# Performance work log

Hardware: AMD Instinct MI355X
Metric: run time of the kernel (lower is better)

Reference implementation:

```python
import jax, jax.numpy as jnp
import numpy as np

N_ATOMS = 30000
N_PAIRS = 1200000
N_BASIS = 7
N_RADIAL = 5
N_SPECIES = 119
R_MIN = 0.5
R_MAX = 6.0
UNITS = (512, 512)
BOX = 6.0  # Angstrom box edge so many pairs fall inside the cutoff
N_FEAT = 360  # gaussian-moment feature count for n_radial=5

# static triangular index sets (fully symmetric contractions)
_TRI2_I, _TRI2_J = np.triu_indices(N_RADIAL)
_TRI3 = np.array([(i, j, k) for i in range(N_RADIAL)
                  for j in range(i, N_RADIAL)
                  for k in range(j, N_RADIAL)], dtype=np.int32)


def setup_inputs() -> dict:
    key = jax.random.key(0)
    ks = jax.random.split(key, 8)
    R = jax.random.uniform(ks[0], (N_ATOMS, 3), jnp.float32) * BOX
    Z = jax.random.randint(ks[1], (N_ATOMS,), 0, N_SPECIES, dtype=jnp.int32)
    idx = jax.random.randint(ks[2], (2, N_PAIRS), 0, N_ATOMS, dtype=jnp.int32)
    W_radial = jax.random.normal(ks[3], (N_SPECIES, N_SPECIES, N_RADIAL, N_BASIS), jnp.float32) / np.sqrt(N_BASIS)
    w1 = jax.random.normal(ks[4], (N_FEAT, UNITS[0]), jnp.float32) / np.sqrt(N_FEAT)
    b1 = jnp.zeros((UNITS[0],), jnp.float32)
    w2 = jax.random.normal(ks[5], (UNITS[0], UNITS[1]), jnp.float32) / np.sqrt(UNITS[0])
    b2 = jnp.zeros((UNITS[1],), jnp.float32)
    w3 = jax.random.normal(ks[6], (UNITS[1], 1), jnp.float32) / np.sqrt(UNITS[1])
    b3 = jnp.zeros((1,), jnp.float32)
    scale = 2.0 * jnp.ones((N_SPECIES, 1), jnp.float32)
    shift = 1.0 * jnp.ones((N_SPECIES, 1), jnp.float32)
    return dict(R=R, Z=Z, idx=idx, W_radial=W_radial, w1=w1, b1=b1,
                w2=w2, b2=b2, w3=w3, b3=b3, scale=scale, shift=shift)


def _descriptor(R, Z, idx, W_radial):
    idx_i, idx_j = idx[0], idx[1]
    # pairwise displacement (free-space displacement fn)
    dr_vec = R[idx_j] - R[idx_i]                                  # [P,3]
    dr = jnp.sqrt(jnp.sum(dr_vec * dr_vec, axis=-1) + 1e-12)      # [P]
    dn = dr_vec / (dr + 1e-5)[:, None]                            # unit vectors [P,3]

    # gaussian radial basis
    betta = N_BASIS ** 2 / R_MAX ** 2
    rad_norm = (2.0 * betta / np.pi) ** 0.25
    shifts = R_MIN + (R_MAX - R_MIN) / N_BASIS * jnp.arange(N_BASIS, dtype=jnp.float32)
    basis = rad_norm * jnp.exp(-betta * (dr[:, None] - shifts) ** 2)  # [P,B]

    # cosine cutoff and per species-pair embedding of the basis
    cutoff = 0.5 * (jnp.cos(jnp.pi * dr / R_MAX) + 1.0) * (dr < R_MAX)
    coeffs = W_radial[Z[idx_i], Z[idx_j]]                          # [P,K,B] irregular gather
    radial = jnp.einsum('pkb,pb->pk', coeffs, basis)               # [P,K]
    radial = radial * (cutoff / np.sqrt(N_BASIS))[:, None]

    seg = lambda x: jax.ops.segment_sum(x, idx_i, num_segments=N_ATOMS)
    # geometric moments of order 0..3
    m0 = seg(radial)                                               # [A,K]
    m1 = seg(radial[:, :, None] * dn[:, None, :])                  # [A,K,3]
    dn2 = dn[:, :, None] * dn[:, None, :]                          # [P,3,3]
    m2 = seg(radial[:, :, None, None] * dn2[:, None])              # [A,K,3,3]
    dn3 = dn2[:, :, :, None] * dn[:, None, None, :]                # [P,3,3,3]
    m3 = seg(radial[:, :, None, None, None] * dn3[:, None])        # [A,K,3,3,3]

    # gaussian-moment invariant contractions
    c1 = jnp.einsum('ari,asi->ars', m1, m1)
    c2 = jnp.einsum('arij,asij->ars', m2, m2)
    c3 = jnp.einsum('arijk,asijk->ars', m3, m3)
    c4 = jnp.einsum('arij,asik,atjk->arst', m2, m2, m2)
    c5 = jnp.einsum('ari,asj,atij->arst', m1, m1, m2)
    c6 = jnp.einsum('arijk,asijl,atkl->arst', m3, m3, m2)
    c7 = jnp.einsum('arijk,asij,atk->arst', m3, m2, m1)

    A = m0.shape[0]
    gm = jnp.concatenate([
        m0,
        c1[:, _TRI2_I, _TRI2_J],
        c2[:, _TRI2_I, _TRI2_J],
        c3[:, _TRI2_I, _TRI2_J],
        c4[:, _TRI3[:, 0], _TRI3[:, 1], _TRI3[:, 2]],
        c5[:, _TRI2_I, _TRI2_J, :].reshape(A, -1),
        c6[:, _TRI2_I, _TRI2_J, :].reshape(A, -1),
        c7.reshape(A, -1),
    ], axis=-1)                                                    # [A,360]
    return gm


def reference(R, Z, idx, W_radial, w1, b1, w2, b2, w3, b3, scale, shift):
    gm = _descriptor(R, Z, idx, W_radial)
    h = jax.nn.swish(gm @ w1 + b1)
    h = jax.nn.swish(h @ w2 + b2)
    h = h @ w3 + b3                                                # [A,1]
    return scale[Z] * h + shift[Z]
```

## Files before the change

kernel.cpp:

```cpp
#include <hip/hip_runtime.h>

#define NA      30000
#define MPAD    30080
#define NPAIRS  1200000
#define NB      7
#define NK      5
#define NSP     119
#define NFEAT   360
#define KP1     384
#define NU      512
#define WROWH   40
#define MAXSLOT 120
#define PSTRIDE 128
#define NBK     118
#define BCAP    11520
#define PPB     4688
#define NTILE   235

#define BETTA      1.3611111111111112f
#define RADNORM    0.96481348f
#define SHIFT_STEP 0.7857142857142857f
#define PI_OVER_R  0.5235987755982988f
#define INV_SQRT7  0.3779644730092272f
#define RMAXV      6.0f
#define TCOEF      2.138888888888889f

typedef __attribute__((ext_vector_type(8))) short bf16x8;
typedef __attribute__((ext_vector_type(4))) float f32x4;
typedef __attribute__((ext_vector_type(2))) float f32x2;
typedef __attribute__((ext_vector_type(4))) unsigned int u32x4;
typedef _Float16 h16x2 __attribute__((ext_vector_type(2)));

__device__ __forceinline__ unsigned short f2b(float x) {
    unsigned u = __float_as_uint(x);
    unsigned r = u + 0x7FFF + ((u >> 16) & 1);
    return (unsigned short)(r >> 16);
}

__global__ __launch_bounds__(256)
void k_part(const int* __restrict__ idx, const int* __restrict__ Z,
            int* __restrict__ gcur, int* __restrict__ part) {
    __shared__ int hist[NBK];
    __shared__ int base[NBK];
    int tid = threadIdx.x;
    for (int b = tid; b < NBK; b += 256) hist[b] = 0;
    __syncthreads();
    int p0 = blockIdx.x * PPB;
    int p1 = min(p0 + PPB, NPAIRS);
    for (int p = p0 + tid; p < p1; p += 256)
        atomicAdd(&hist[idx[p] >> 8], 1);
    __syncthreads();
    for (int b = tid; b < NBK; b += 256) {
        base[b] = atomicAdd(&gcur[b], hist[b]);
        hist[b] = 0;
    }
    __syncthreads();
    for (int p = p0 + tid; p < p1; p += 256) {
        int i = idx[p];
        int b = i >> 8;
        int j = idx[NPAIRS + p];
        int zj = Z[j];
        int off = base[b] + atomicAdd(&hist[b], 1);
        if (off < BCAP)
            part[b * BCAP + off] = ((i & 255) << 22) | (zj << 15) | j;
    }
}

__global__ __launch_bounds__(256)
void k_csr(const int* __restrict__ part, const int* __restrict__ gcnt,
           int* __restrict__ counts, int* __restrict__ plist) {
    __shared__ int lp[128 * MAXSLOT];
    __shared__ int lc[128];
    int tid = threadIdx.x;
    int lane = tid & 63, wave = tid >> 6;
    int w = blockIdx.x;
    int cb = w >> 1;
    int par = w & 1;
    for (int t = tid; t < 128; t += 256) lc[t] = 0;
    __syncthreads();
    int n = min(gcnt[cb], BCAP);
    for (int e = tid; e < n; e += 256) {
        int v = part[cb * BCAP + e];
        int iloc = v >> 22;
        if ((iloc >> 7) == par) {
            int i7 = iloc & 127;
            int r = atomicAdd(&lc[i7], 1);
            if (r < MAXSLOT) lp[i7 * MAXSLOT + r] = v & 0x3FFFFF;
        }
    }
    __syncthreads();
    for (int t = tid; t < 128; t += 256) {
        int a = w * 128 + t;
        if (a < NA) counts[a] = min(lc[t], MAXSLOT);
    }
    for (int rr = 0; rr < 32; rr++) {
        int row = wave * 32 + rr;
        int a = w * 128 + row;
        if (a < NA) {
            int n_r = min(lc[row], MAXSLOT);
            for (int c = lane; c < n_r; c += 64)
                plist[(size_t)a * PSTRIDE + c] = lp[row * MAXSLOT + c];
        }
    }
}

#define PREP_W   (NSP*NSP*WROWH)
#define PREP_R   NA
#define PREP_W1  (NU*KP1)
#define PREP_W2  (NU*NU)
#define PREP_TOT (PREP_W + PREP_R + PREP_W1 + PREP_W2)
__global__ void k_prep(const float* __restrict__ W, const float* __restrict__ R,
                       const float* __restrict__ w1, const float* __restrict__ w2,
                       unsigned short* __restrict__ Wp, float* __restrict__ Rp,
                       unsigned short* __restrict__ w1T, unsigned short* __restrict__ w2T,
                       int* __restrict__ gcur, float* __restrict__ out) {
    int i = blockIdx.x * blockDim.x + threadIdx.x;
    if (i < 128) gcur[i] = 0;
    if (i < NA) out[i] = 0.f;
    if (i < PREP_W) {
        int row = i / WROWH, e = i - row * WROWH;
        int k = e >> 3, b = e & 7;
        float v = (b < 7) ? W[row * (NK * NB) + k * NB + b] : 0.f;
        ((_Float16*)Wp)[i] = (_Float16)v;
        return;
    }
    i -= PREP_W;
    if (i < PREP_R) {
        f32x4 v = {R[3*i], R[3*i+1], R[3*i+2], 0.f};
        *(f32x4*)&Rp[4*i] = v;
        return;
    }
    i -= PREP_R;
    if (i < PREP_W1) {
        int c = i / KP1, kp = i - c * KP1;
        w1T[i] = (kp < NFEAT) ? f2b(w1[kp * NU + c]) : (unsigned short)0;
        return;
    }
    i -= PREP_W1;
    if (i < PREP_W2) {
        int c = i >> 9, kp = i & 511;
        w2T[i] = f2b(w2[kp * NU + c]);
    }
}

#define LDM(comp) M[(comp) * 65]

__device__ __forceinline__ void do_c5(const float* M, unsigned short* STrow,
                                      int r, int s, int foff) {
    const int S2[3][3] = {{0,1,2},{1,3,4},{2,4,5}};
    float m1r[3], m1q[3];
#pragma unroll
    for (int i = 0; i < 3; i++) m1r[i] = LDM(r*20+1+i);
#pragma unroll
    for (int i = 0; i < 3; i++) m1q[i] = LDM(s*20+1+i);
    float pre[9];
#pragma unroll
    for (int i = 0; i < 3; i++)
#pragma unroll
        for (int j = 0; j < 3; j++) pre[i*3+j] = m1r[i] * m1q[j];
    for (int t = 0; t < 5; t++) {
        float m2t[6];
#pragma unroll
        for (int u = 0; u < 6; u++) m2t[u] = LDM(t*20+4+u);
        float v = 0.f;
#pragma unroll
        for (int i = 0; i < 3; i++)
#pragma unroll
            for (int j = 0; j < 3; j++)
                v += pre[i*3+j] * m2t[S2[i][j]];
        STrow[foff + t] = f2b(v);
    }
}

__device__ __forceinline__ void do_c6(const float* M, unsigned short* STrow,
                                      int r, int s, int foff) {
    const int S2[3][3] = {{0,1,2},{1,3,4},{2,4,5}};
    const int S3[3][3][3] = {
        {{0,1,2},{1,3,4},{2,4,5}},
        {{1,3,4},{3,6,7},{4,7,8}},
        {{2,4,5},{4,7,8},{5,8,9}}
    };
    float m3r[10];
#pragma unroll
    for (int u = 0; u < 10; u++) m3r[u] = LDM(r*20+10+u);
    float m2q[6];
#pragma unroll
    for (int u = 0; u < 6; u++) m2q[u] = LDM(s*20+4+u);
    float U0 = 0.f, U1 = 0.f, U2 = 0.f;
#pragma unroll
    for (int i = 0; i < 3; i++)
#pragma unroll
        for (int j = 0; j < 3; j++) {
            float ww = m2q[S2[i][j]];
            U0 += m3r[S3[i][j][0]] * ww;
            U1 += m3r[S3[i][j][1]] * ww;
            U2 += m3r[S3[i][j][2]] * ww;
        }
    for (int t = 0; t < 5; t++) {
        float v = U0 * LDM(t*20+1) + U1 * LDM(t*20+2) + U2 * LDM(t*20+3);
        STrow[foff + t] = f2b(v);
    }
}

__device__ __forceinline__ void do_c7(const float* M, unsigned short* STrow,
                                      int r, int s, int foff) {
    const int S2[3][3] = {{0,1,2},{1,3,4},{2,4,5}};
    const int S3[3][3][3] = {
        {{0,1,2},{1,3,4},{2,4,5}},
        {{1,3,4},{3,6,7},{4,7,8}},
        {{2,4,5},{4,7,8},{5,8,9}}
    };
    float m3r[10], m3q[10];
#pragma unroll
    for (int u = 0; u < 10; u++) m3r[u] = LDM(r*20+10+u);
#pragma unroll
    for (int u = 0; u < 10; u++) m3q[u] = LDM(s*20+10+u);
    float T[3][3];
#pragma unroll
    for (int k = 0; k < 3; k++)
#pragma unroll
        for (int l = 0; l < 3; l++) {
            float v = 0.f;
#pragma unroll
            for (int i = 0; i < 3; i++)
#pragma unroll
                for (int j = 0; j < 3; j++)
                    v += m3r[S3[i][j][k]] * m3q[S3[i][j][l]];
            T[k][l] = v;
        }
    for (int t = 0; t < 5; t++) {
        float m2t[6];
#pragma unroll
        for (int u = 0; u < 6; u++) m2t[u] = LDM(t*20+4+u);
        float v = 0.f;
#pragma unroll
        for (int k = 0; k < 3; k++)
#pragma unroll
            for (int l = 0; l < 3; l++)
                v += T[k][l] * m2t[S2[k][l]];
        STrow[foff + t] = f2b(v);
    }
}

__global__ __launch_bounds__(512, 2)
void k_momcon(const float* __restrict__ Rp, const int* __restrict__ Z,
              const unsigned short* __restrict__ WpH, const int* __restrict__ counts,
              const int* __restrict__ plist, unsigned short* __restrict__ gmB) {
    __shared__ float MS[100 * 65];
    __shared__ __align__(4) unsigned short ST[64 * 242];
    int tid = threadIdx.x;
    int g = tid >> 3, q = tid & 7;
    int a0 = blockIdx.x * 64;
    int a = a0 + g;

    if (a < NA) {
        f32x4 ri = *(const f32x4*)&Rp[4*a];
        int Zi = Z[a];
        f32x2 acc[50];
#pragma unroll
        for (int u = 0; u < 50; u++) acc[u] = (f32x2){0.f, 0.f};
        int cnt = min(counts[a], MAXSLOT);
        const int* prow = plist + (size_t)a * PSTRIDE;

        const float DCH[6] = {0.14812156f, 0.027590652f, 0.0051393300f,
                              0.00095730500f, 0.00017831700f, 3.3215300e-05f};

        int pk0 = prow[q & 127];
        int pk1 = prow[(q + 8) & 127];
        int j0c = min(pk0 & 0x7FFF, NA - 1);
        f32x4 rj = *(const f32x4*)&Rp[4 * j0c];

        for (int t = q; t < cnt; t += 8) {
            int pk2 = prow[(t + 16) & 127];
            int j1c = min(pk1 & 0x7FFF, NA - 1);
            f32x4 rjn = *(const f32x4*)&Rp[4 * j1c];

            int Zj = (pk0 >> 15) & 0x7F;
            const u32x4* wv = (const u32x4*)(WpH + (size_t)(Zi * NSP + Zj) * WROWH);
            u32x4 wv0 = wv[0], wv1 = wv[1], wv2 = wv[2], wv3 = wv[3], wv4 = wv[4];
            unsigned wu[20];
#pragma unroll
            for (int c = 0; c < 4; c++) {
                wu[c]      = wv0[c];
                wu[4 + c]  = wv1[c];
                wu[8 + c]  = wv2[c];
                wu[12 + c] = wv3[c];
                wu[16 + c] = wv4[c];
            }

            float dx = rj.x - ri.x, dy = rj.y - ri.y, dz = rj.z - ri.z;
            float d2 = dx*dx + dy*dy + dz*dz + 1e-12f;
            float dr = sqrtf(d2);
            float inv = 1.0f / (dr + 1e-5f);
            float nx = dx*inv, ny = dy*inv, nz = dz*inv;

            float t0 = dr - 0.5f;
            float bb[NB];
            bb[0] = RADNORM * __expf(-BETTA * t0 * t0);
            float Tg = __expf(TCOEF * dr);
#pragma unroll
            for (int b = 0; b < 6; b++) bb[b+1] = bb[b] * Tg * DCH[b];

            float cut = (dr < RMAXV) ? 0.5f * (__cosf(PI_OVER_R * dr) + 1.0f) : 0.0f;
            cut *= INV_SQRT7;

            h16x2 bp[4];
            bp[0] = (h16x2){(_Float16)bb[0], (_Float16)bb[1]};
            bp[1] = (h16x2){(_Float16)bb[2], (_Float16)bb[3]};
            bp[2] = (h16x2){(_Float16)bb[4], (_Float16)bb[5]};
            bp[3] = (h16x2){(_Float16)bb[6], (_Float16)0.0f};

            float rad[NK];
#pragma unroll
            for (int k = 0; k < NK; k++) {
                float s = 0.f;
#if __has_builtin(__builtin_amdgcn_fdot2)
#pragma unroll
                for (int c = 0; c < 4; c++)
                    s = __builtin_amdgcn_fdot2(
                        __builtin_bit_cast(h16x2, wu[k*4 + c]), bp[c], s, false);
#else
#pragma unroll
                for (int c = 0; c < 4; c++) {
                    h16x2 w = __builtin_bit_cast(h16x2, wu[k*4 + c]);
                    s += (float)w.x * (float)bp[c].x + (float)w.y * (float)bp[c].y;
                }
#endif
                rad[k] = s * cut;
            }

            float gg[20];
            gg[0] = 1.f; gg[1] = nx; gg[2] = ny; gg[3] = nz;
            gg[4] = nx*nx; gg[5] = nx*ny; gg[6] = nx*nz; gg[7] = ny*ny; gg[8] = ny*nz; gg[9] = nz*nz;
            gg[10] = gg[4]*nx; gg[11] = gg[4]*ny; gg[12] = gg[4]*nz; gg[13] = gg[5]*ny; gg[14] = gg[5]*nz;
            gg[15] = gg[6]*nz; gg[16] = gg[7]*ny; gg[17] = gg[7]*nz; gg[18] = gg[8]*nz; gg[19] = gg[9]*nz;
            f32x2 g2[10];
#pragma unroll
            for (int u = 0; u < 10; u++) g2[u] = (f32x2){gg[2*u], gg[2*u+1]};
#pragma unroll
            for (int k = 0; k < NK; k++) {
                f32x2 rk = (f32x2){rad[k], rad[k]};
#pragma unroll
                for (int u = 0; u < 10; u++)
                    acc[k*10 + u] += rk * g2[u];
            }
            pk0 = pk1; pk1 = pk2; rj = rjn;
        }
#pragma unroll
        for (int u = 0; u < 50; u++) {
            f32x2 v = acc[u];
            double d = __builtin_bit_cast(double, v);
            d = __shfl_xor(d, 1);
            v += __builtin_bit_cast(f32x2, d);
            d = __builtin_bit_cast(double, v);
            d = __shfl_xor(d, 2);
            v += __builtin_bit_cast(f32x2, d);
            d = __builtin_bit_cast(double, v);
            d = __shfl_xor(d, 4);
            v += __builtin_bit_cast(f32x2, d);
            acc[u] = v;
        }
        if (q == 0) {
#pragma unroll
            for (int u = 0; u < 50; u++) {
                MS[(2*u)     * 65 + g] = acc[u].x;
                MS[(2*u + 1) * 65 + g] = acc[u].y;
            }
        }
    }
    __syncthreads();

    int lane = tid & 63, wave = tid >> 6;
    const float* M = MS + lane;
    unsigned short* STrow = ST + lane * 242;

    if (wave == 0) {
        for (int k = 0; k < 5; k++) STrow[k] = f2b(LDM(k * 20));
        int f = 5;
        for (int r = 0; r < 5; r++)
            for (int s = r; s < 5; s++) {
                float v = 0.f;
#pragma unroll
                for (int i = 0; i < 3; i++) v += LDM(r*20+1+i) * LDM(s*20+1+i);
                STrow[f++] = f2b(v);
            }
        const float W2U[6] = {1,2,2,1,2,1};
        for (int r = 0; r < 5; r++)
            for (int s = r; s < 5; s++) {
                float v = 0.f;
#pragma unroll
                for (int u = 0; u < 6; u++) v += W2U[u] * LDM(r*20+4+u) * LDM(s*20+4+u);
                STrow[f++] = f2b(v);
            }
        const float W3U[10] = {1,3,3,3,6,3,1,3,3,1};
        for (int r = 0; r < 5; r++)
            for (int s = r; s < 5; s++) {
                float v = 0.f;
#pragma unroll
                for (int u = 0; u < 10; u++) v += W3U[u] * LDM(r*20+10+u) * LDM(s*20+10+u);
                STrow[f++] = f2b(v);
            }
        do_c7(M, STrow, 3, 4, 160 + 13*5);
        do_c7(M, STrow, 4, 4, 160 + 14*5);
    } else if (wave == 1 || wave == 2) {
        const int S2[3][3] = {{0,1,2},{1,3,4},{2,4,5}};
        int e0 = (wave == 1) ? 0 : 18, e1 = (wave == 1) ? 18 : 35;
        int e = 0;
        for (int r = 0; r < 5; r++)
            for (int s = r; s < 5; s++)
                for (int t = s; t < 5; t++) {
                    if (e >= e0 && e < e1) {
                        float m2r[6], m2q[6], m2t[6];
#pragma unroll
                        for (int u = 0; u < 6; u++) m2r[u] = LDM(r*20+4+u);
#pragma unroll
                        for (int u = 0; u < 6; u++) m2q[u] = LDM(s*20+4+u);
#pragma unroll
                        for (int u = 0; u < 6; u++) m2t[u] = LDM(t*20+4+u);
                        float v = 0.f;
#pragma unroll
                        for (int i = 0; i < 3; i++)
#pragma unroll
                            for (int j = 0; j < 3; j++)
#pragma unroll
                                for (int k = 0; k < 3; k++)
                                    v += m2r[S2[i][j]] * m2q[S2[i][k]] * m2t[S2[j][k]];
                        STrow[50 + e] = f2b(v);
                    }
                    e++;
                }
    } else if (wave == 3) {
        int p = 0;
        for (int r = 0; r < 5; r++)
            for (int s = r; s < 5; s++) {
                if (p < 8) do_c5(M, STrow, r, s, 85 + p*5);
                p++;
            }
        do_c7(M, STrow, 3, 3, 160 + 12*5);
    } else if (wave == 4) {
        int p = 0;
        for (int r = 0; r < 5; r++)
            for (int s = r; s < 5; s++) {
                if (p >= 8) do_c5(M, STrow, r, s, 85 + p*5);
                p++;
            }
        do_c6(M, STrow, 0, 0, 235);
    } else {
        int pc0 = (wave - 5) * 4;
        int p = 0;
        for (int r = 0; r < 5; r++)
            for (int s = r; s < 5; s++) {
                if (p >= pc0 && p < pc0 + 4) do_c7(M, STrow, r, s, 160 + p*5);
                p++;
            }
    }
    __syncthreads();
    for (int e = tid; e < 64 * 120; e += 512) {
        int row = e / 120, c = e - row * 120;
        if (a0 + row < NA)
            *(unsigned int*)&gmB[(size_t)(a0 + row) * KP1 + 2*c] =
                *(const unsigned int*)&ST[row * 242 + 2*c];
    }
    __syncthreads();

    {
        int g0 = 1 + wave * 3;
        for (int gi = 0; gi < 3; gi++) {
            int gr = g0 + gi;
            int r = gr / 5, s = gr - r * 5;
            do_c6(M, STrow, r, s, 235 + gr*5 - 240);
        }
        if (wave == 0) {
            for (int z = 360; z < 384; z++) STrow[z - 240] = 0;
        }
    }
    __syncthreads();
    for (int e = tid; e < 64 * 72; e += 512) {
        int row = e / 72, c = e - row * 72;
        if (a0 + row < NA)
            *(unsigned int*)&gmB[(size_t)(a0 + row) * KP1 + 240 + 2*c] =
                *(const unsigned int*)&ST[row * 242 + 2*c];
    }
}

__device__ __forceinline__ void stage8(const unsigned short* gp, unsigned short* lp) {
    __builtin_amdgcn_global_load_lds(
        (const __attribute__((address_space(1))) unsigned int*)gp,
        (__attribute__((address_space(3))) unsigned int*)lp, 16, 0, 0);
}

template<int KPAD, int MODE>
__global__ __launch_bounds__(256) void k_mfma(const unsigned short* __restrict__ A,
                                              const unsigned short* __restrict__ B,
                                              const float* __restrict__ bias,
                                              const float* __restrict__ w3,
                                              void* __restrict__ outp) {
    __shared__ __align__(16) unsigned char SMEM[35072];
    unsigned short* As = (unsigned short*)SMEM;
    unsigned short* Bs = (unsigned short*)(SMEM + 16384);
    float* red = (float*)(SMEM + 32768);
    int tid = threadIdx.x;
    int lane = tid & 63, wave = tid >> 6;
    int wm = wave >> 1, wn = wave & 1;
    int quad = lane >> 4, l16 = lane & 15;
    int lrow = lane >> 3;
    int lchk = lane & 7;

    for (int t = 0; t < 2; t++) {
        int atile = blockIdx.y * 2 + t;
        if (atile >= NTILE) break;
        int rowA0, rowB0;
        if (MODE == 1) { rowA0 = atile * 128;      rowB0 = blockIdx.x * 128; }
        else           { rowA0 = blockIdx.x * 128; rowB0 = atile * 128; }

        f32x4 acc[4][4];
        f32x4 zero = {0.f, 0.f, 0.f, 0.f};
#pragma unroll
        for (int i = 0; i < 4; i++)
#pragma unroll
            for (int j = 0; j < 4; j++) acc[i][j] = zero;

        for (int k0 = 0; k0 < KPAD; k0 += 64) {
            __syncthreads();
#pragma unroll
            for (int i = 0; i < 4; i++) {
                int r = wave * 32 + i * 8 + lrow;
                int gc = lchk ^ (r & 7);
                stage8(A + (size_t)(rowA0 + r) * KPAD + k0 + gc * 8, &As[(wave * 32 + i * 8) * 64]);
            }
#pragma unroll
            for (int i = 0; i < 4; i++) {
                int r = wave * 32 + i * 8 + lrow;
                int gc = lchk ^ (r & 7);
                stage8(B + (size_t)(rowB0 + r) * KPAD + k0 + gc * 8, &Bs[(wave * 32 + i * 8) * 64]);
            }
            __syncthreads();
#pragma unroll
            for (int s = 0; s < 2; s++) {
                bf16x8 af[4], bfr[4];
#pragma unroll
                for (int mt = 0; mt < 4; mt++) {
                    int r = wm * 64 + mt * 16 + l16;
                    af[mt] = *(const bf16x8*)&As[r * 64 + (((s * 4 + quad) ^ (r & 7)) * 8)];
                }
#pragma unroll
                for (int nt = 0; nt < 4; nt++) {
                    int r = wn * 64 + nt * 16 + l16;
                    bfr[nt] = *(const bf16x8*)&Bs[r * 64 + (((s * 4 + quad) ^ (r & 7)) * 8)];
                }
#pragma unroll
                for (int mt = 0; mt < 4; mt++)
#pragma unroll
                    for (int nt = 0; nt < 4; nt++)
                        acc[mt][nt] = __builtin_amdgcn_mfma_f32_16x16x32_bf16(
                            af[mt], bfr[nt], acc[mt][nt], 0, 0, 0);
            }
        }

        if (MODE == 1) {
            __syncthreads();
            unsigned short* Ot = (unsigned short*)SMEM;
#pragma unroll
            for (int nt = 0; nt < 4; nt++) {
                int c_loc = wn * 64 + nt * 16 + l16;
                float b = bias[rowB0 + c_loc];
#pragma unroll
                for (int mt = 0; mt < 4; mt++) {
#pragma unroll
                    for (int reg = 0; reg < 4; reg++) {
                        int a_loc = wm * 64 + mt * 16 + quad * 4 + reg;
                        float v = acc[mt][nt][reg] + b;
                        Ot[a_loc * 136 + c_loc] = f2b(v / (1.f + __expf(-v)));
                    }
                }
            }
            __syncthreads();
            unsigned short* O = (unsigned short*)outp;
            int half = lane >> 5, l32 = lane & 31;
#pragma unroll
            for (int it = 0; it < 16; it++) {
                int rloc = wave * 32 + it * 2 + half;
                int a = rowA0 + rloc;
                unsigned long long d = *(const unsigned long long*)&Ot[rloc * 136 + l32 * 4];
                if (a < NA)
                    *(unsigned long long*)&O[(size_t)a * NU + rowB0 + l32 * 4] = d;
            }
        } else {
            float pn[4] = {0.f, 0.f, 0.f, 0.f};
#pragma unroll
            for (int mt = 0; mt < 4; mt++) {
#pragma unroll
                for (int reg = 0; reg < 4; reg++) {
                    int c = rowA0 + wm * 64 + mt * 16 + quad * 4 + reg;
                    float b = bias[c];
                    float w3c = w3[c];
#pragma unroll
                    for (int nt = 0; nt < 4; nt++) {
                        float v = acc[mt][nt][reg] + b;
                        pn[nt] += w3c * (v / (1.f + __expf(-v)));
                    }
                }
            }
#pragma unroll
            for (int nt = 0; nt < 4; nt++) {
                pn[nt] += __shfl_xor(pn[nt], 16);
                pn[nt] += __shfl_xor(pn[nt], 32);
            }
            __syncthreads();
            if (quad == 0) {
#pragma unroll
                for (int nt = 0; nt < 4; nt++)
                    red[((wm * 2 + wn) * 4 + nt) * 16 + l16] = pn[nt];
            }
            __syncthreads();
            if (tid < 128) {
                int wn2 = tid >> 6, nt2 = (tid >> 4) & 3, lb = tid & 15;
                float s = red[((0 * 2 + wn2) * 4 + nt2) * 16 + lb]
                        + red[((1 * 2 + wn2) * 4 + nt2) * 16 + lb];
                int a = rowB0 + wn2 * 64 + nt2 * 16 + lb;
                if (a < NA) atomicAdd((float*)outp + a, s);
            }
        }
    }
}

__global__ void k_finish(float* __restrict__ out, const float* __restrict__ b3,
                         const int* __restrict__ Z, const float* __restrict__ scale,
                         const float* __restrict__ shift) {
    int a = blockIdx.x * blockDim.x + threadIdx.x;
    if (a >= NA) return;
    int z = Z[a];
    out[a] = scale[z] * (out[a] + b3[0]) + shift[z];
}

extern "C" void kernel_launch(void* const* d_in, const int* in_sizes, int n_in,
                              void* d_out, int out_size, void* d_ws, size_t ws_size,
                              hipStream_t stream) {
    const float* R    = (const float*)d_in[0];
    const int*   Z    = (const int*)  d_in[1];
    const int*   idx  = (const int*)  d_in[2];
    const float* Wr   = (const float*)d_in[3];
    const float* w1   = (const float*)d_in[4];
    const float* b1   = (const float*)d_in[5];
    const float* w2   = (const float*)d_in[6];
    const float* b2   = (const float*)d_in[7];
    const float* w3   = (const float*)d_in[8];
    const float* b3   = (const float*)d_in[9];
    const float* scale= (const float*)d_in[10];
    const float* shift= (const float*)d_in[11];
    float* out = (float*)d_out;
    char* ws = (char*)d_ws;

    int*            gcur   = (int*)  (ws + 0);
    int*            counts = (int*)  (ws + 512);
    int*            part   = (int*)  (ws + 120576);
    int*            plist  = (int*)  (ws + 5558016);
    unsigned short* gmB    = (unsigned short*)(ws + 32918016);
    unsigned short* w1T    = (unsigned short*)(ws + 56019456);
    unsigned short* w2T    = (unsigned short*)(ws + 56412672);
    unsigned short* h1B    = (unsigned short*)(ws + 56936960);
    unsigned short* WpH    = (unsigned short*)(ws + 87738880);
    float*          Rpad   = (float*)(ws + 89778064);

    k_prep   <<<(PREP_TOT + 255) / 256, 256, 0, stream>>>(Wr, R, w1, w2, WpH, Rpad,
                                                          w1T, w2T, gcur, out);
    k_part   <<<256, 256, 0, stream>>>(idx, Z, gcur, part);
    k_csr    <<<235, 256, 0, stream>>>(part, gcur, counts, plist);
    k_momcon <<<(NA + 63) / 64, 512, 0, stream>>>(Rpad, Z, WpH, counts, plist, gmB);

    k_mfma<KP1, 1><<<dim3(NU / 128, 118), 256, 0, stream>>>(gmB, w1T, b1, nullptr, (void*)h1B);
    k_mfma<NU,  2><<<dim3(NU / 128, 118), 256, 0, stream>>>(w2T, h1B, b2, w3, (void*)out);

    k_finish<<<(NA + 255) / 256, 256, 0, stream>>>(out, b3, Z, scale, shift);
}
```

Baseline: 247.6 us.

## Flatten per-atom pair loops into block-wide load-balanced pair stage via LDS

Restructures the moment-accumulation kernel into two phases: all 512 threads first compute radial and direction values for a flattened list of the block's pairs (prefix-summed offsets plus a row-of lookup) and store them in shared memory, then each 8-thread atom group reads those values and accumulates its moments. This targets load imbalance across atoms whose neighbour counts differ, and divergence in the gather-heavy radial phase. In exchange it adds extra syncthreads, a scan, and LDS round-trips. It also caps the pairs per block at 3264, so a block whose neighbour total exceeds that cap would silently drop pairs.

```diff
diff --git a/kernel.cpp b/kernel.cpp
--- a/kernel.cpp
+++ b/kernel.cpp
@@ -16,6 +16,8 @@
 #define BCAP    11520
 #define PPB     4688
 #define NTILE   235
+#define PDCAP   3264
+#define PDHALF  1632
 
 #define BETTA      1.3611111111111112f
 #define RADNORM    0.96481348f
@@ -246,36 +248,69 @@
 void k_momcon(const float* __restrict__ Rp, const int* __restrict__ Z,
               const unsigned short* __restrict__ WpH, const int* __restrict__ counts,
               const int* __restrict__ plist, unsigned short* __restrict__ gmB) {
-    __shared__ float MS[100 * 65];
-    __shared__ __align__(4) unsigned short ST[64 * 242];
+    __shared__ __align__(16) unsigned char LDSM[57040];
+    float* pd = (float*)LDSM;
+    float* MS = (float*)LDSM;
+    unsigned short* ST = (unsigned short*)(LDSM + 26000);
+    unsigned char* rowof = LDSM + 52224;
+    int* off = (int*)(LDSM + 55488);
+    f32x4* Rb = (f32x4*)(LDSM + 55760);
+    int* Zb = (int*)(LDSM + 56784);
+
     int tid = threadIdx.x;
+    int a0 = blockIdx.x * 64;
+
+    if (tid < 64) {
+        int aa = a0 + tid;
+        int c = (aa < NA) ? min(counts[aa], MAXSLOT) : 0;
+        int v = c;
+#pragma unroll
+        for (int d = 1; d < 64; d <<= 1) {
+            int o = __shfl_up(v, d);
+            if (tid >= d) v += o;
+        }
+        off[tid + 1] = v;
+        if (tid == 0) off[0] = 0;
+        if (aa < NA) {
+            Rb[tid] = *(const f32x4*)&Rp[4 * aa];
+            Zb[tid] = Z[aa];
+        } else {
+            Rb[tid] = (f32x4){0.f, 0.f, 0.f, 0.f};
+            Zb[tid] = 0;
+        }
+    }
+    __syncthreads();
+    int tot = min(off[64], PDCAP);
+    {
+        int r = tid >> 3, q8 = tid & 7;
+        int e0r = off[r], e1r = min(off[r + 1], PDCAP);
+        for (int e = e0r + q8; e < e1r; e += 8) rowof[e] = (unsigned char)r;
+    }
+    __syncthreads();
+
     int g = tid >> 3, q = tid & 7;
-    int a0 = blockIdx.x * 64;
-    int a = a0 + g;
-
-    if (a < NA) {
-        f32x4 ri = *(const f32x4*)&Rp[4*a];
-        int Zi = Z[a];
-        f32x2 acc[50];
-#pragma unroll
-        for (int u = 0; u < 50; u++) acc[u] = (f32x2){0.f, 0.f};
-        int cnt = min(counts[a], MAXSLOT);
-        const int* prow = plist + (size_t)a * PSTRIDE;
-
-        const float DCH[6] = {0.14812156f, 0.027590652f, 0.0051393300f,
-                              0.00095730500f, 0.00017831700f, 3.3215300e-05f};
-
-        int pk0 = prow[q & 127];
-        int pk1 = prow[(q + 8) & 127];
-        int j0c = min(pk0 & 0x7FFF, NA - 1);
-        f32x4 rj = *(const f32x4*)&Rp[4 * j0c];
-
-        for (int t = q; t < cnt; t += 8) {
-            int pk2 = prow[(t + 16) & 127];
-            int j1c = min(pk1 & 0x7FFF, NA - 1);
-            f32x4 rjn = *(const f32x4*)&Rp[4 * j1c];
-
-            int Zj = (pk0 >> 15) & 0x7F;
+    int gbase = off[g];
+    int gcnt = off[g + 1] - gbase;
+    f32x2 acc[50];
+#pragma unroll
+    for (int u = 0; u < 50; u++) acc[u] = (f32x2){0.f, 0.f};
+
+    const float DCH[6] = {0.14812156f, 0.027590652f, 0.0051393300f,
+                          0.00095730500f, 0.00017831700f, 3.3215300e-05f};
+
+    for (int batch = 0; batch < 2; batch++) {
+        int e0 = batch * PDHALF;
+        int e1 = min(tot, e0 + PDHALF);
+
+        for (int e = e0 + tid; e < e1; e += 512) {
+            int r = rowof[e];
+            int slot = e - off[r];
+            int pk = plist[(size_t)(a0 + r) * PSTRIDE + slot];
+            int j = pk & 0x7FFF, Zj = (pk >> 15) & 0x7F;
+            f32x4 ri = Rb[r];
+            int Zi = Zb[r];
+            f32x4 rj = *(const f32x4*)&Rp[4 * j];
+
             const u32x4* wv = (const u32x4*)(WpH + (size_t)(Zi * NSP + Zj) * WROWH);
             u32x4 wv0 = wv[0], wv1 = wv[1], wv2 = wv[2], wv3 = wv[3], wv4 = wv[4];
             unsigned wu[20];
@@ -329,43 +364,73 @@
                 rad[k] = s * cut;
             }
 
-            float gg[20];
-            gg[0] = 1.f; gg[1] = nx; gg[2] = ny; gg[3] = nz;
-            gg[4] = nx*nx; gg[5] = nx*ny; gg[6] = nx*nz; gg[7] = ny*ny; gg[8] = ny*nz; gg[9] = nz*nz;
-            gg[10] = gg[4]*nx; gg[11] = gg[4]*ny; gg[12] = gg[4]*nz; gg[13] = gg[5]*ny; gg[14] = gg[5]*nz;
-            gg[15] = gg[6]*nz; gg[16] = gg[7]*ny; gg[17] = gg[7]*nz; gg[18] = gg[8]*nz; gg[19] = gg[9]*nz;
-            f32x2 g2[10];
-#pragma unroll
-            for (int u = 0; u < 10; u++) g2[u] = (f32x2){gg[2*u], gg[2*u+1]};
-#pragma unroll
-            for (int k = 0; k < NK; k++) {
-                f32x2 rk = (f32x2){rad[k], rad[k]};
-#pragma unroll
-                for (int u = 0; u < 10; u++)
-                    acc[k*10 + u] += rk * g2[u];
-            }
-            pk0 = pk1; pk1 = pk2; rj = rjn;
-        }
+            int el = e - e0;
+            pd[0 * PDHALF + el] = rad[0];
+            pd[1 * PDHALF + el] = rad[1];
+            pd[2 * PDHALF + el] = rad[2];
+            pd[3 * PDHALF + el] = rad[3];
+            pd[4 * PDHALF + el] = rad[4];
+            pd[5 * PDHALF + el] = nx;
+            pd[6 * PDHALF + el] = ny;
+            pd[7 * PDHALF + el] = nz;
+        }
+        __syncthreads();
+
+        {
+            int tlo = max(0, e0 - gbase);
+            int thi = min(gcnt, e1 - gbase);
+            int t = tlo + ((q - tlo) & 7);
+            for (; t < thi; t += 8) {
+                int el = (gbase + t) - e0;
+                float rad[NK];
+                rad[0] = pd[0 * PDHALF + el];
+                rad[1] = pd[1 * PDHALF + el];
+                rad[2] = pd[2 * PDHALF + el];
+                rad[3] = pd[3 * PDHALF + el];
+                rad[4] = pd[4 * PDHALF + el];
+                float nx = pd[5 * PDHALF + el];
+                float ny = pd[6 * PDHALF + el];
+                float nz = pd[7 * PDHALF + el];
+
+                float gg[20];
+                gg[0] = 1.f; gg[1] = nx; gg[2] = ny; gg[3] = nz;
+                gg[4] = nx*nx; gg[5] = nx*ny; gg[6] = nx*nz; gg[7] = ny*ny; gg[8] = ny*nz; gg[9] = nz*nz;
+                gg[10] = gg[4]*nx; gg[11] = gg[4]*ny; gg[12] = gg[4]*nz; gg[13] = gg[5]*ny; gg[14] = gg[5]*nz;
+                gg[15] = gg[6]*nz; gg[16] = gg[7]*ny; gg[17] = gg[7]*nz; gg[18] = gg[8]*nz; gg[19] = gg[9]*nz;
+                f32x2 g2[10];
+#pragma unroll
+                for (int u = 0; u < 10; u++) g2[u] = (f32x2){gg[2*u], gg[2*u+1]};
+#pragma unroll
+                for (int k = 0; k < NK; k++) {
+                    f32x2 rk = (f32x2){rad[k], rad[k]};
+#pragma unroll
+                    for (int u = 0; u < 10; u++)
+                        acc[k*10 + u] += rk * g2[u];
+                }
+            }
+        }
+        __syncthreads();
+    }
+
+#pragma unroll
+    for (int u = 0; u < 50; u++) {
+        f32x2 v = acc[u];
+        double d = __builtin_bit_cast(double, v);
+        d = __shfl_xor(d, 1);
+        v += __builtin_bit_cast(f32x2, d);
+        d = __builtin_bit_cast(double, v);
+        d = __shfl_xor(d, 2);
+        v += __builtin_bit_cast(f32x2, d);
+        d = __builtin_bit_cast(double, v);
+        d = __shfl_xor(d, 4);
+        v += __builtin_bit_cast(f32x2, d);
+        acc[u] = v;
+    }
+    if (q == 0) {
 #pragma unroll
         for (int u = 0; u < 50; u++) {
-            f32x2 v = acc[u];
-            double d = __builtin_bit_cast(double, v);
-            d = __shfl_xor(d, 1);
-            v += __builtin_bit_cast(f32x2, d);
-            d = __builtin_bit_cast(double, v);
-            d = __shfl_xor(d, 2);
-            v += __builtin_bit_cast(f32x2, d);
-            d = __builtin_bit_cast(double, v);
-            d = __shfl_xor(d, 4);
-            v += __builtin_bit_cast(f32x2, d);
-            acc[u] = v;
-        }
-        if (q == 0) {
-#pragma unroll
-            for (int u = 0; u < 50; u++) {
-                MS[(2*u)     * 65 + g] = acc[u].x;
-                MS[(2*u + 1) * 65 + g] = acc[u].y;
-            }
+            MS[(2*u)     * 65 + g] = acc[u].x;
+            MS[(2*u + 1) * 65 + g] = acc[u].y;
         }
     }
     __syncthreads();
@@ -404,12 +469,12 @@
         do_c7(M, STrow, 4, 4, 160 + 14*5);
     } else if (wave == 1 || wave == 2) {
         const int S2[3][3] = {{0,1,2},{1,3,4},{2,4,5}};
-        int e0 = (wave == 1) ? 0 : 18, e1 = (wave == 1) ? 18 : 35;
+        int e0w = (wave == 1) ? 0 : 18, e1w = (wave == 1) ? 18 : 35;
         int e = 0;
         for (int r = 0; r < 5; r++)
             for (int s = r; s < 5; s++)
                 for (int t = s; t < 5; t++) {
-                    if (e >= e0 && e < e1) {
+                    if (e >= e0w && e < e1w) {
                         float m2r[6], m2q[6], m2t[6];
 #pragma unroll
                         for (int u = 0; u < 6; u++) m2r[u] = LDM(r*20+4+u);
```

After: 252.2 us. About the same (+1.9%).
